# Optimization experiments

Hardware: AMD Instinct MI355X
Metric: run time of the kernel (lower is better)

The kernel has to match this reference:

```python
import jax, jax.numpy as jnp
import numpy as np

B, S, W = 64, 128, 16
E, H = 256, 512
WV, CV, NC = 50000, 128, 20


def _lstm(x, lens, Wih, Whh, b):
    """Masked LSTM over padded sequences.
    x: [N,T,D], lens: [N] int. Returns (ys [N,T,Hd] zeroed past lens, h_last [N,Hd]).
    Gate layout [i,f,g,o] as in PyTorch; b = b_ih + b_hh fused.
    """
    N, T, _ = x.shape
    Hd = Whh.shape[1]

    def step(carry, inp):
        h, c = carry
        xt, t = inp
        z = xt @ Wih.T + h @ Whh.T + b  # [N,4Hd]
        i, f, g, o = jnp.split(z, 4, axis=-1)
        c_new = jax.nn.sigmoid(f) * c + jax.nn.sigmoid(i) * jnp.tanh(g)
        h_new = jax.nn.sigmoid(o) * jnp.tanh(c_new)
        m = (t < lens)[:, None]
        h = jnp.where(m, h_new, h)  # freeze state past sequence end (packed semantics)
        c = jnp.where(m, c_new, c)
        return (h, c), jnp.where(m, h, 0.0)

    h0 = jnp.zeros((N, Hd), x.dtype)
    (h, _), ys = jax.lax.scan(step, (h0, h0), (jnp.swapaxes(x, 0, 1), jnp.arange(T)))
    return jnp.swapaxes(ys, 0, 1), h


def _rev_pad(x, lens):
    """Reverse each sequence within its valid length; padding stays in place."""
    T = x.shape[1]
    t = jnp.arange(T)[None, :]
    idx = jnp.where(t < lens[:, None], lens[:, None] - 1 - t, t)
    return jnp.take_along_axis(x, idx[:, :, None], axis=1)


def setup_inputs() -> dict:
    key = jax.random.key(0)
    ks = jax.random.split(key, 16)
    sc = 0.05
    words = jax.random.randint(ks[0], (B, S), 0, WV)
    words_num = jax.random.randint(ks[1], (B,), 1, S + 1)
    chars = jax.random.randint(ks[2], (B, S, W), 0, CV)
    char_lens = jax.random.randint(ks[3], (B, S), 1, W + 1)
    word_emb = jax.random.normal(ks[4], (WV, E)) * sc
    char_emb = jax.random.normal(ks[5], (CV, E)) * sc
    l0_Wih = jax.random.normal(ks[6], (2, 4 * H, E)) * sc
    l0_Whh = jax.random.normal(ks[7], (2, 4 * H, H)) * sc
    l0_b = jax.random.normal(ks[8], (2, 4 * H)) * sc
    l1_Wih = jax.random.normal(ks[9], (2, 4 * H, 2 * H)) * sc
    l1_Whh = jax.random.normal(ks[10], (2, 4 * H, H)) * sc
    l1_b = jax.random.normal(ks[11], (2, 4 * H)) * sc
    c_Wih = jax.random.normal(ks[12], (4 * (2 * H), E)) * sc
    c_Whh = jax.random.normal(ks[13], (4 * (2 * H), 2 * H)) * sc
    c_b = jax.random.normal(ks[14], (4 * (2 * H),)) * sc
    lin_W = jax.random.normal(ks[15], (NC, 2 * H)) * sc
    lin_b = jnp.zeros((NC,))
    return dict(words=words, words_num=words_num, chars=chars, char_lens=char_lens,
                word_emb=word_emb, char_emb=char_emb,
                l0_Wih=l0_Wih, l0_Whh=l0_Whh, l0_b=l0_b,
                l1_Wih=l1_Wih, l1_Whh=l1_Whh, l1_b=l1_b,
                c_Wih=c_Wih, c_Whh=c_Whh, c_b=c_b,
                lin_W=lin_W, lin_b=lin_b)


def reference(words, words_num, chars, char_lens, word_emb, char_emb,
              l0_Wih, l0_Whh, l0_b, l1_Wih, l1_Whh, l1_b,
              c_Wih, c_Whh, c_b, lin_W, lin_b):
    # word path: embedding + 2-layer bidirectional LSTM (packed -> masked)
    h = word_emb[words]  # [B,S,E]
    for Wih, Whh, b in ((l0_Wih, l0_Whh, l0_b), (l1_Wih, l1_Whh, l1_b)):
        fwd, _ = _lstm(h, words_num, Wih[0], Whh[0], b[0])
        bwd, _ = _lstm(_rev_pad(h, words_num), words_num, Wih[1], Whh[1], b[1])
        h = jnp.concatenate([fwd, _rev_pad(bwd, words_num)], axis=-1)  # [B,S,2H]

    # char path: one batched LSTM over all B*S words (collapses per-sentence loop)
    b_, s_, w_ = chars.shape
    ce = char_emb[chars.reshape(b_ * s_, w_)]  # [B*S,W,E]
    _, hc = _lstm(ce, char_lens.reshape(b_ * s_), c_Wih, c_Whh, c_b)  # final h_n [B*S,2H]
    y = hc.reshape(b_, s_, -1)
    valid = (jnp.arange(s_)[None, :] < words_num[:, None])[..., None]
    y = jnp.where(valid, y, 0.0)  # pad_sequence pads missing words with zeros

    return (h + y) @ lin_W.T + lin_b  # [B,S,NC]
```

## Files before the change

### kernel.cpp

```cpp
#include <hip/hip_runtime.h>
#include <stdint.h>

#define SLEN 128
#define NW 8192
#define WCH 16
#define EDIM 256
#define HDIM 512
#define G4 2048
#define CH 1024
#define CG 4096
#define NCLS 20

typedef __attribute__((ext_vector_type(4))) float f32x4;
typedef __attribute__((ext_vector_type(8))) short s16x8;

__device__ __forceinline__ ushort f2b(float f){
  uint32_t u = __float_as_uint(f);
  return (ushort)((u + 0x7FFFu + ((u>>16)&1u)) >> 16);
}
__device__ __forceinline__ float b2f(ushort s){ return __uint_as_float(((uint32_t)s)<<16); }
__device__ __forceinline__ float sigf(float x){ return 1.f/(1.f+__expf(-x)); }
__device__ __forceinline__ float tanhf_(float x){
  float t = fminf(fmaxf(2.f*x,-30.f),30.f);
  float e = __expf(t);
  return (e-1.f)/(e+1.f);
}

__device__ __forceinline__ void gl16(const ushort* g, ushort* l){
  __builtin_amdgcn_global_load_lds((const __attribute__((address_space(1))) uint32_t*)g,
                                   (__attribute__((address_space(3))) uint32_t*)l, 16, 0, 0);
}

__global__ void k_fill(uint32_t* __restrict__ p, uint32_t v, int n){
  int i = blockIdx.x*256 + threadIdx.x;
  if (i < n) p[i] = v;
}

__global__ void k_cvt(const float* __restrict__ s, ushort* __restrict__ d, int n){
  int i = blockIdx.x*256 + threadIdx.x;
  if (i < n) d[i] = f2b(s[i]);
}

__global__ void k_cwhhp(const float* __restrict__ s, ushort* __restrict__ d){
  int i = blockIdx.x*256 + threadIdx.x;
  int dr = i >> 10, k = i & 1023;
  int nb = dr >> 7, w7 = dr & 127;
  int g = w7 >> 5, wn = (w7>>4)&1, hl = w7&15;
  int h = nb*32 + wn*16 + hl;
  d[i] = f2b(s[(size_t)(g*1024 + h)*1024 + k]);
}

__global__ void k_wwhhp(const float* __restrict__ s, ushort* __restrict__ d){
  int i = blockIdx.x*256 + threadIdx.x;
  int dr = i >> 9, k = i & 511;
  int dir = dr >> 11; int r = dr & 2047;
  int y = r >> 7, w7 = r & 127;
  int g = w7 >> 5, wn = (w7>>4)&1, hl = w7&15;
  int h = y*32 + wn*16 + hl;
  d[i] = f2b(s[((size_t)dir*2048 + g*512 + h)*512 + k]);
}

__global__ void k_emb(const int* __restrict__ words, const float* __restrict__ we,
                      ushort* __restrict__ d){
  int i = blockIdx.x*256 + threadIdx.x;
  int w = i >> 8, e = i & 255;
  d[i] = f2b(we[(size_t)words[w]*EDIM + e]);
}

__global__ void k_cproj(const float* __restrict__ cemb, const float* __restrict__ cwih,
                        const float* __restrict__ cb, float* __restrict__ out){
  int i = blockIdx.x*256 + threadIdx.x;
  int c = i >> 12, p = i & 4095;
  int nb = p >> 7, w7 = p & 127;
  int g = w7>>5, wn = (w7>>4)&1, hl = w7&15;
  int j = g*1024 + nb*32 + wn*16 + hl;
  const float* a = cemb + (size_t)c*EDIM;
  const float* b = cwih + (size_t)j*EDIM;
  float acc = cb[j];
  for (int k=0;k<EDIM;k+=4){
    float4 av = *(const float4*)&a[k]; float4 bv = *(const float4*)&b[k];
    acc += av.x*bv.x + av.y*bv.y + av.z*bv.z + av.w*bv.w;
  }
  out[i] = acc;
}

__global__ void k_hist(const int* __restrict__ wn, const int* __restrict__ cl,
                       int* __restrict__ cnt17){
  int w = blockIdx.x*256 + threadIdx.x; if (w >= NW) return;
  int b = w >> 7, s = w & 127;
  if (s < wn[b]) atomicAdd(&cnt17[cl[w]], 1);
}

__global__ void k_scan(const int* __restrict__ cnt17, int* __restrict__ cnt_step,
                       int* __restrict__ cur){
  if (threadIdx.x==0 && blockIdx.x==0){
    cnt_step[16] = 0;
    for (int t=15;t>=0;t--) cnt_step[t] = cnt_step[t+1] + cnt17[t+1];
    for (int l=1;l<=16;l++) cur[l] = cnt_step[l];
  }
}

__global__ void k_scatter(const int* __restrict__ wn, const int* __restrict__ cl,
                          const int* __restrict__ chars, int* __restrict__ cur,
                          int* __restrict__ inv, int* __restrict__ chperm){
  int w = blockIdx.x*256 + threadIdx.x; if (w >= NW) return;
  int b = w >> 7, s = w & 127;
  if (s < wn[b]){
    int len = cl[w];
    int pos = atomicAdd(&cur[len], 1);
    inv[w] = pos;
    for (int j=0;j<WCH;j++) chperm[pos*WCH + j] = chars[w*WCH + j];
  }
}

template<int EPI>
__global__ __launch_bounds__(256) void k_gemm(
    const ushort* __restrict__ A, int ldA,
    const ushort* __restrict__ Bm, int ldB, size_t bStrideZ,
    ushort* __restrict__ outX, const float* __restrict__ bias,
    size_t oStrideZ, size_t biasStrideZ, int K,
    const int* __restrict__ cnt_step, int tstep,
    const int* __restrict__ chperm, const float* __restrict__ cproj,
    float* __restrict__ ccell, ushort* __restrict__ hcdst)
{
  int cntv = 0;
  if (EPI==1){ cntv = cnt_step[tstep]; if ((int)(blockIdx.x*128) >= cntv) return; }
  __shared__ __align__(16) ushort As[128*64];
  __shared__ __align__(16) ushort Bs[128*64];
  int tid = threadIdx.x, wid = tid>>6, lane = tid&63;
  int wm = wid>>1, wn = wid&1;
  int l15 = lane&15, l4 = lane>>4;
  const ushort* Ab = A + (size_t)blockIdx.x*128*ldA;
  const ushort* Bb = Bm + (size_t)blockIdx.z*bStrideZ + (size_t)blockIdx.y*128*ldB;
  f32x4 acc[4][4];
  #pragma unroll
  for (int i=0;i<4;i++)
    #pragma unroll
    for (int j=0;j<4;j++) acc[i][j] = f32x4{0.f,0.f,0.f,0.f};

  for (int k0=0; k0<K; k0+=64){
    #pragma unroll
    for (int i=0;i<4;i++){
      int fcb = (i*4 + wid)*64;
      int fc = fcb + lane;
      int row = fc>>3, cp = fc&7, c = cp ^ (row&7);
      gl16(Ab + (size_t)row*ldA + k0 + c*8, As + fcb*8);
    }
    #pragma unroll
    for (int i=0;i<4;i++){
      int fcb = (i*4 + wid)*64;
      int fc = fcb + lane;
      int row = fc>>3, cp = fc&7, c = cp ^ (row&7);
      gl16(Bb + (size_t)row*ldB + k0 + c*8, Bs + fcb*8);
    }
    __syncthreads();
    #pragma unroll
    for (int kw=0; kw<2; kw++){
      s16x8 af[4], bfr[4];
      #pragma unroll
      for (int mf=0; mf<4; mf++){
        int r = wm*64 + mf*16 + l15;
        int slot = (kw*4 + l4) ^ (r&7);
        af[mf] = *(const s16x8*)&As[r*64 + slot*8];
      }
      #pragma unroll
      for (int nf=0; nf<4; nf++){
        int r = (EPI==1) ? (nf*32 + wn*16 + l15) : (wn*64 + nf*16 + l15);
        int slot = (kw*4 + l4) ^ (r&7);
        bfr[nf] = *(const s16x8*)&Bs[r*64 + slot*8];
      }
      #pragma unroll
      for (int mf=0; mf<4; mf++)
        #pragma unroll
        for (int nf=0; nf<4; nf++)
          acc[mf][nf] = __builtin_amdgcn_mfma_f32_16x16x32_bf16(af[mf], bfr[nf], acc[mf][nf], 0,0,0);
    }
    __syncthreads();
  }

  if (EPI==0){
    ushort* op = outX + blockIdx.z*oStrideZ;
    const float* bp = bias + blockIdx.z*biasStrideZ;
    #pragma unroll
    for (int mf=0; mf<4; mf++){
      #pragma unroll
      for (int r=0;r<4;r++){
        int row = blockIdx.x*128 + wm*64 + mf*16 + l4*4 + r;
        #pragma unroll
        for (int nf=0;nf<4;nf++){
          int col = blockIdx.y*128 + wn*64 + nf*16 + l15;
          op[(size_t)row*G4 + col] = f2b(acc[mf][nf][r] + bp[col]);
        }
      }
    }
  } else {
    int hb = blockIdx.y*32 + wn*16 + l15;
    #pragma unroll
    for (int mf=0; mf<4; mf++){
      #pragma unroll
      for (int r=0;r<4;r++){
        int row = blockIdx.x*128 + wm*64 + mf*16 + l4*4 + r;
        if (row < cntv){
          int cid = chperm[row*WCH + tstep];
          const float* cp = cproj + (size_t)cid*CG + blockIdx.y*128 + wn*16 + l15;
          float zi = acc[mf][0][r] + cp[0];
          float zf = acc[mf][1][r] + cp[32];
          float zg = acc[mf][2][r] + cp[64];
          float zo = acc[mf][3][r] + cp[96];
          size_t ix = (size_t)row*CH + hb;
          float c = ccell[ix];
          float cn = sigf(zf)*c + sigf(zi)*tanhf_(zg);
          ccell[ix] = cn;
          hcdst[ix] = f2b(sigf(zo)*tanhf_(cn));
        }
      }
    }
  }
}

__global__ __launch_bounds__(256) void k_wstep(
    const ushort* __restrict__ hsrc,
    ushort* __restrict__ hdst,
    float* __restrict__ cst,
    const ushort* __restrict__ X,
    const ushort* __restrict__ Wp,
    const int* __restrict__ lens,
    ushort* __restrict__ outcat,
    int t)
{
  __shared__ __align__(16) ushort As[64*64];
  __shared__ __align__(16) ushort Bs[128*64];
  int tid = threadIdx.x, wid = tid>>6, lane = tid&63;
  int l15 = lane&15, l4 = lane>>4;
  int y = blockIdx.x;
  int dir = blockIdx.y;
  const ushort* Ab = hsrc + (size_t)dir*64*512;
  const ushort* Bb = Wp + ((size_t)dir*2048 + (size_t)y*128)*512;
  f32x4 acc[8];
  #pragma unroll
  for (int n=0;n<8;n++) acc[n] = f32x4{0.f,0.f,0.f,0.f};

  for (int k0=0; k0<512; k0+=64){
    #pragma unroll
    for (int i=0;i<2;i++){
      int fcb = (i*4 + wid)*64;
      int fc = fcb + lane;
      int row = fc>>3, cp = fc&7, c = cp ^ (row&7);
      gl16(Ab + (size_t)row*512 + k0 + c*8, As + fcb*8);
    }
    #pragma unroll
    for (int i=0;i<4;i++){
      int fcb = (i*4 + wid)*64;
      int fc = fcb + lane;
      int row = fc>>3, cp = fc&7, c = cp ^ (row&7);
      gl16(Bb + (size_t)row*512 + k0 + c*8, Bs + fcb*8);
    }
    __syncthreads();
    #pragma unroll
    for (int kw=0; kw<2; kw++){
      s16x8 af;
      {
        int r = wid*16 + l15;
        int slot = (kw*4 + l4) ^ (r&7);
        af = *(const s16x8*)&As[r*64 + slot*8];
      }
      #pragma unroll
      for (int nf=0; nf<8; nf++){
        int r = nf*16 + l15;
        int slot = (kw*4 + l4) ^ (r&7);
        s16x8 bfr = *(const s16x8*)&Bs[r*64 + slot*8];
        acc[nf] = __builtin_amdgcn_mfma_f32_16x16x32_bf16(af, bfr, acc[nf], 0,0,0);
      }
    }
    __syncthreads();
  }

  int b0 = wid*16 + l4*4;
  int lenv[4], posv[4];
  #pragma unroll
  for (int r=0;r<4;r++){
    int len = lens[b0+r];
    lenv[r] = len;
    posv[r] = dir ? (len-1-t) : t;
  }
  #pragma unroll
  for (int wn=0;wn<2;wn++){
    int h = y*32 + wn*16 + l15;
    #pragma unroll
    for (int r=0;r<4;r++){
      int b = b0 + r;
      size_t hix = ((size_t)dir*64 + b)*512 + h;
      ushort hnew;
      if (t < lenv[r]){
        size_t xbase = ((size_t)dir*NW + (size_t)b*SLEN + posv[r])*G4 + h;
        float zi = acc[0+wn][r] + b2f(X[xbase]);
        float zf = acc[2+wn][r] + b2f(X[xbase + 512]);
        float zg = acc[4+wn][r] + b2f(X[xbase + 1024]);
        float zo = acc[6+wn][r] + b2f(X[xbase + 1536]);
        size_t cix = ((size_t)dir*512 + h)*64 + b;
        float c = cst[cix];
        float cn = sigf(zf)*c + sigf(zi)*tanhf_(zg);
        cst[cix] = cn;
        float hv = sigf(zo)*tanhf_(cn);
        hnew = f2b(hv);
        outcat[((size_t)b*SLEN + posv[r])*1024 + dir*HDIM + h] = hnew;
      } else {
        hnew = hsrc[hix];
      }
      hdst[hix] = hnew;
    }
  }
}

__global__ void k_gather(const ushort* __restrict__ hc0, const ushort* __restrict__ hc1,
                         const int* __restrict__ inv, const int* __restrict__ cl,
                         ushort* __restrict__ ycat){
  int i = blockIdx.x*256 + threadIdx.x;
  if (i >= NW*128) return;
  int w = i >> 7, seg = i & 127;
  int iv = inv[w];
  ulonglong2 z; z.x = 0; z.y = 0;
  if (iv >= 0){
    const ushort* src = (((cl[w]-1)&1) ? hc0 : hc1) + (size_t)iv*CH + seg*8;
    z = *(const ulonglong2*)src;
  }
  *(ulonglong2*)(ycat + (size_t)w*CH + seg*8) = z;
}

__global__ __launch_bounds__(256) void k_final(
    const ushort* __restrict__ h1cat, const ushort* __restrict__ ycat,
    const float* __restrict__ lw, const float* __restrict__ lb,
    float* __restrict__ out)
{
  int i = blockIdx.x*256 + threadIdx.x;
  if (i >= NW*NCLS) return;
  int w = i / NCLS, o = i - w*NCLS;
  const ushort* hr = h1cat + (size_t)w*1024;
  const ushort* yr = ycat  + (size_t)w*1024;
  const float* wr = lw + (size_t)o*1024;
  float acc = lb[o];
  for (int k=0;k<1024;k+=4){
    float4 wv = *(const float4*)&wr[k];
    ushort4 a4 = *(const ushort4*)&hr[k];
    ushort4 b4 = *(const ushort4*)&yr[k];
    acc += (b2f(a4.x)+b2f(b4.x))*wv.x + (b2f(a4.y)+b2f(b4.y))*wv.y
         + (b2f(a4.z)+b2f(b4.z))*wv.z + (b2f(a4.w)+b2f(b4.w))*wv.w;
  }
  out[i] = acc;
}

extern "C" void kernel_launch(void* const* d_in, const int* in_sizes, int n_in,
                              void* d_out, int out_size, void* d_ws, size_t ws_size,
                              hipStream_t stream)
{
  const int*   words = (const int*)d_in[0];
  const int*   wnum  = (const int*)d_in[1];
  const int*   chars = (const int*)d_in[2];
  const int*   clens = (const int*)d_in[3];
  const float* wemb  = (const float*)d_in[4];
  const float* cemb  = (const float*)d_in[5];
  const float* l0Wih = (const float*)d_in[6];
  const float* l0Whh = (const float*)d_in[7];
  const float* l0b   = (const float*)d_in[8];
  const float* l1Wih = (const float*)d_in[9];
  const float* l1Whh = (const float*)d_in[10];
  const float* l1b   = (const float*)d_in[11];
  const float* cWih  = (const float*)d_in[12];
  const float* cWhh  = (const float*)d_in[13];
  const float* cb    = (const float*)d_in[14];
  const float* linW  = (const float*)d_in[15];
  const float* linb  = (const float*)d_in[16];
  float* out = (float*)d_out;

  char* base = (char*)d_ws;
  const size_t MB = (size_t)1<<20;
  ushort* hc0    = (ushort*)(base);
  ushort* hc1    = (ushort*)(base + 16*MB);
  float*  ccell  = (float*) (base + 32*MB);
  ushort* X      = (ushort*)(base);
  ushort* cwp    = (ushort*)(base + 64*MB);
  ushort* l1w    = (ushort*)(base + 64*MB);
  float*  cproj  = (float*) (base + 72*MB);
  int*    chperm = (int*)   (base + 74*MB);
  ushort* embw   = (ushort*)(base + 72*MB);
  ushort* w1p    = (ushort*)(base + 72*MB);
  ushort* ycat   = (ushort*)(base + 76*MB);
  ushort* h0cat  = (ushort*)(base + 92*MB);
  ushort* h1cat  = (ushort*)(base + 92*MB);
  ushort* l0w    = (ushort*)(base + 108*MB);
  ushort* w0p    = (ushort*)(base + 110*MB);
  ushort* hA     = (ushort*)(base + 114*MB);
  ushort* hB     = (ushort*)(base + 114*MB + 128*1024);
  float*  cw     = (float*) (base + 114*MB + 256*1024);
  int*    inv    = (int*)   (base + 114*MB + 512*1024);
  int*    cnt17  = (int*)   (base + 114*MB + 544*1024);
  int*    cntstep= (int*)   (base + 114*MB + 545*1024);
  int*    cur    = (int*)   (base + 114*MB + 546*1024);

  k_fill<<<1, 256, 0, stream>>>((uint32_t*)cnt17, 0u, 17);
  k_fill<<<(NW+255)/256, 256, 0, stream>>>((uint32_t*)inv, 0xFFFFFFFFu, NW);
  k_fill<<<(NW*CH/2+255)/256, 256, 0, stream>>>((uint32_t*)hc0, 0u, NW*CH/2);
  k_fill<<<(NW*CH+255)/256, 256, 0, stream>>>((uint32_t*)ccell, 0u, NW*CH);
  k_cwhhp<<<(CG*CH)/256, 256, 0, stream>>>(cWhh, cwp);
  k_cproj<<<(128*CG)/256, 256, 0, stream>>>(cemb, cWih, cb, cproj);
  k_hist<<<NW/256, 256, 0, stream>>>(wnum, clens, cnt17);
  k_scan<<<1, 1, 0, stream>>>(cnt17, cntstep, cur);
  k_scatter<<<NW/256, 256, 0, stream>>>(wnum, clens, chars, cur, inv, chperm);

  for (int t=0;t<WCH;t++){
    const ushort* hs = (t&1)? hc1 : hc0;
    ushort*       hd = (t&1)? hc0 : hc1;
    k_gemm<1><<<dim3(64,32,1), 256, 0, stream>>>(hs, CH, cwp, CH, 0,
        nullptr, nullptr, 0, 0, CH,
        cntstep, t, chperm, cproj, ccell, hd);
  }
  k_gather<<<(NW*128+255)/256, 256, 0, stream>>>(hc0, hc1, inv, clens, ycat);

  k_cvt<<<(2*G4*EDIM+255)/256, 256, 0, stream>>>(l0Wih, l0w, 2*G4*EDIM);
  k_cvt<<<(2*G4*1024+255)/256, 256, 0, stream>>>(l1Wih, l1w, 2*G4*1024);
  k_wwhhp<<<(2*G4*HDIM)/256, 256, 0, stream>>>(l0Whh, w0p);
  k_emb<<<(NW*EDIM)/256, 256, 0, stream>>>(words, wemb, embw);
  k_fill<<<(NW*512+255)/256, 256, 0, stream>>>((uint32_t*)h0cat, 0u, NW*512);
  k_fill<<<(32768+255)/256, 256, 0, stream>>>((uint32_t*)hA, 0u, 32768);
  k_fill<<<(65536+255)/256, 256, 0, stream>>>((uint32_t*)cw, 0u, 65536);

  k_gemm<0><<<dim3(64,16,2), 256, 0, stream>>>(embw, EDIM, l0w, EDIM, (size_t)G4*EDIM,
      X, l0b, (size_t)NW*G4, (size_t)G4, EDIM,
      nullptr, 0, nullptr, nullptr, nullptr, nullptr);

  k_wwhhp<<<(2*G4*HDIM)/256, 256, 0, stream>>>(l1Whh, w1p);

  for (int t=0;t<SLEN;t++){
    const ushort* hs = (t&1)? hB : hA;
    ushort*       hd = (t&1)? hA : hB;
    k_wstep<<<dim3(16,2), 256, 0, stream>>>(hs, hd, cw, X, w0p, wnum, h0cat, t);
  }

  k_fill<<<(32768+255)/256, 256, 0, stream>>>((uint32_t*)hA, 0u, 32768);
  k_fill<<<(65536+255)/256, 256, 0, stream>>>((uint32_t*)cw, 0u, 65536);

  k_gemm<0><<<dim3(64,16,2), 256, 0, stream>>>(h0cat, 1024, l1w, 1024, (size_t)G4*1024,
      X, l1b, (size_t)NW*G4, (size_t)G4, 1024,
      nullptr, 0, nullptr, nullptr, nullptr, nullptr);

  k_fill<<<(NW*512+255)/256, 256, 0, stream>>>((uint32_t*)h1cat, 0u, NW*512);

  for (int t=0;t<SLEN;t++){
    const ushort* hs = (t&1)? hB : hA;
    ushort*       hd = (t&1)? hA : hB;
    k_wstep<<<dim3(16,2), 256, 0, stream>>>(hs, hd, cw, X, w1p, wnum, h1cat, t);
  }

  k_final<<<(NW*NCLS+255)/256, 256, 0, stream>>>(h1cat, ycat, linW, linb, out);
}
```

Before: 4.837 ms.

## Replace per-step word LSTM launches with persistent kernel and grid barrier

Each word-LSTM layer now runs as one persistent 32-block kernel instead of 128 separate launches. Each block keeps its 128-row slice of Whh resident in LDS (128 KB), holds the cell state in registers, and synchronises the 16 blocks of each direction through an atomic counter barrier in global memory after every timestep. This removes launch overhead and the repeated reload of the weights per step. The price is a spin-wait barrier that depends on all 32 blocks being co-resident, plus high LDS use per block.

Result: faster. 4.432 ms (-8.4%).

```diff
diff --git a/kernel.cpp b/kernel.cpp
--- a/kernel.cpp
+++ b/kernel.cpp
@@ -218,97 +218,117 @@
   }
 }
 
-__global__ __launch_bounds__(256) void k_wstep(
-    const ushort* __restrict__ hsrc,
-    ushort* __restrict__ hdst,
-    float* __restrict__ cst,
+__global__ __launch_bounds__(256) void k_wrec(
+    ushort* __restrict__ hbuf,
     const ushort* __restrict__ X,
     const ushort* __restrict__ Wp,
     const int* __restrict__ lens,
     ushort* __restrict__ outcat,
-    int t)
+    int* __restrict__ bar)
 {
+  __shared__ __align__(16) ushort Ws[8*128*64];
   __shared__ __align__(16) ushort As[64*64];
-  __shared__ __align__(16) ushort Bs[128*64];
   int tid = threadIdx.x, wid = tid>>6, lane = tid&63;
   int l15 = lane&15, l4 = lane>>4;
-  int y = blockIdx.x;
-  int dir = blockIdx.y;
-  const ushort* Ab = hsrc + (size_t)dir*64*512;
-  const ushort* Bb = Wp + ((size_t)dir*2048 + (size_t)y*128)*512;
-  f32x4 acc[8];
+  int y = blockIdx.x & 15, dir = blockIdx.x >> 4;
+  const ushort* Wb = Wp + ((size_t)dir*2048 + (size_t)y*128)*512;
+
   #pragma unroll
-  for (int n=0;n<8;n++) acc[n] = f32x4{0.f,0.f,0.f,0.f};
-
-  for (int k0=0; k0<512; k0+=64){
-    #pragma unroll
-    for (int i=0;i<2;i++){
-      int fcb = (i*4 + wid)*64;
-      int fc = fcb + lane;
-      int row = fc>>3, cp = fc&7, c = cp ^ (row&7);
-      gl16(Ab + (size_t)row*512 + k0 + c*8, As + fcb*8);
-    }
+  for (int kt=0; kt<8; ++kt)
     #pragma unroll
     for (int i=0;i<4;i++){
       int fcb = (i*4 + wid)*64;
       int fc = fcb + lane;
       int row = fc>>3, cp = fc&7, c = cp ^ (row&7);
-      gl16(Bb + (size_t)row*512 + k0 + c*8, Bs + fcb*8);
-    }
+      gl16(Wb + (size_t)row*512 + kt*64 + c*8, Ws + kt*8192 + fcb*8);
+    }
+  asm volatile("s_waitcnt vmcnt(0)" ::: "memory");
+  __builtin_amdgcn_sched_barrier(0);
+  __builtin_amdgcn_s_barrier();
+
+  int b0 = wid*16 + l4*4;
+  int lenv[4];
+  #pragma unroll
+  for (int r=0;r<4;r++) lenv[r] = lens[b0+r];
+  float  cacc[2][4];
+  ushort hprev[2][4];
+  #pragma unroll
+  for (int wn=0;wn<2;wn++)
+    #pragma unroll
+    for (int r=0;r<4;r++){ cacc[wn][r]=0.f; hprev[wn][r]=0; }
+
+  int* mybar = bar + dir;
+
+  for (int t=0;t<SLEN;t++){
+    const ushort* hsrc = hbuf + ((size_t)((t&1)*2 + dir))*32768;
+    ushort*       hdst = hbuf + ((size_t)((((t&1)^1))*2 + dir))*32768;
+    f32x4 acc[8];
+    #pragma unroll
+    for (int n=0;n<8;n++) acc[n] = f32x4{0.f,0.f,0.f,0.f};
+
+    for (int kt=0; kt<8; ++kt){
+      #pragma unroll
+      for (int i=0;i<2;i++){
+        int fcb = (i*4 + wid)*64;
+        int fc = fcb + lane;
+        int row = fc>>3, cp = fc&7, c = cp ^ (row&7);
+        gl16(hsrc + (size_t)row*512 + kt*64 + c*8, As + fcb*8);
+      }
+      asm volatile("s_waitcnt vmcnt(0)" ::: "memory");
+      __builtin_amdgcn_sched_barrier(0);
+      __builtin_amdgcn_s_barrier();
+      #pragma unroll
+      for (int kw=0; kw<2; kw++){
+        s16x8 af;
+        { int r = wid*16 + l15; int slot = (kw*4 + l4) ^ (r&7);
+          af = *(const s16x8*)&As[r*64 + slot*8]; }
+        #pragma unroll
+        for (int nf=0; nf<8; nf++){
+          int r = nf*16 + l15; int slot = (kw*4 + l4) ^ (r&7);
+          s16x8 bfr = *(const s16x8*)&Ws[kt*8192 + r*64 + slot*8];
+          acc[nf] = __builtin_amdgcn_mfma_f32_16x16x32_bf16(af, bfr, acc[nf], 0,0,0);
+        }
+      }
+      __builtin_amdgcn_s_barrier();
+    }
+
+    #pragma unroll
+    for (int wn=0;wn<2;wn++){
+      int h = y*32 + wn*16 + l15;
+      #pragma unroll
+      for (int r=0;r<4;r++){
+        int b = b0 + r;
+        ushort hnew;
+        if (t < lenv[r]){
+          int pos = dir ? (lenv[r]-1-t) : t;
+          size_t xbase = ((size_t)dir*NW + (size_t)b*SLEN + pos)*G4 + h;
+          float zi = acc[0+wn][r] + b2f(X[xbase]);
+          float zf = acc[2+wn][r] + b2f(X[xbase + 512]);
+          float zg = acc[4+wn][r] + b2f(X[xbase + 1024]);
+          float zo = acc[6+wn][r] + b2f(X[xbase + 1536]);
+          float cn = sigf(zf)*cacc[wn][r] + sigf(zi)*tanhf_(zg);
+          cacc[wn][r] = cn;
+          float hv = sigf(zo)*tanhf_(cn);
+          hnew = f2b(hv);
+          outcat[((size_t)b*SLEN + pos)*1024 + dir*HDIM + h] = hnew;
+        } else {
+          hnew = hprev[wn][r];
+        }
+        hprev[wn][r] = hnew;
+        hdst[(size_t)b*512 + h] = hnew;
+      }
+    }
+
     __syncthreads();
-    #pragma unroll
-    for (int kw=0; kw<2; kw++){
-      s16x8 af;
-      {
-        int r = wid*16 + l15;
-        int slot = (kw*4 + l4) ^ (r&7);
-        af = *(const s16x8*)&As[r*64 + slot*8];
-      }
-      #pragma unroll
-      for (int nf=0; nf<8; nf++){
-        int r = nf*16 + l15;
-        int slot = (kw*4 + l4) ^ (r&7);
-        s16x8 bfr = *(const s16x8*)&Bs[r*64 + slot*8];
-        acc[nf] = __builtin_amdgcn_mfma_f32_16x16x32_bf16(af, bfr, acc[nf], 0,0,0);
-      }
+    if (tid==0){
+      __threadfence();
+      __hip_atomic_fetch_add(mybar, 1, __ATOMIC_RELEASE, __HIP_MEMORY_SCOPE_AGENT);
+      int tgt = 16*(t+1);
+      while (__hip_atomic_load(mybar, __ATOMIC_ACQUIRE, __HIP_MEMORY_SCOPE_AGENT) < tgt)
+        __builtin_amdgcn_s_sleep(8);
+      __threadfence();
     }
     __syncthreads();
-  }
-
-  int b0 = wid*16 + l4*4;
-  int lenv[4], posv[4];
-  #pragma unroll
-  for (int r=0;r<4;r++){
-    int len = lens[b0+r];
-    lenv[r] = len;
-    posv[r] = dir ? (len-1-t) : t;
-  }
-  #pragma unroll
-  for (int wn=0;wn<2;wn++){
-    int h = y*32 + wn*16 + l15;
-    #pragma unroll
-    for (int r=0;r<4;r++){
-      int b = b0 + r;
-      size_t hix = ((size_t)dir*64 + b)*512 + h;
-      ushort hnew;
-      if (t < lenv[r]){
-        size_t xbase = ((size_t)dir*NW + (size_t)b*SLEN + posv[r])*G4 + h;
-        float zi = acc[0+wn][r] + b2f(X[xbase]);
-        float zf = acc[2+wn][r] + b2f(X[xbase + 512]);
-        float zg = acc[4+wn][r] + b2f(X[xbase + 1024]);
-        float zo = acc[6+wn][r] + b2f(X[xbase + 1536]);
-        size_t cix = ((size_t)dir*512 + h)*64 + b;
-        float c = cst[cix];
-        float cn = sigf(zf)*c + sigf(zi)*tanhf_(zg);
-        cst[cix] = cn;
-        float hv = sigf(zo)*tanhf_(cn);
-        hnew = f2b(hv);
-        outcat[((size_t)b*SLEN + posv[r])*1024 + dir*HDIM + h] = hnew;
-      } else {
-        hnew = hsrc[hix];
-      }
-      hdst[hix] = hnew;
-    }
   }
 }
 
@@ -389,9 +409,8 @@
   ushort* h1cat  = (ushort*)(base + 92*MB);
   ushort* l0w    = (ushort*)(base + 108*MB);
   ushort* w0p    = (ushort*)(base + 110*MB);
-  ushort* hA     = (ushort*)(base + 114*MB);
-  ushort* hB     = (ushort*)(base + 114*MB + 128*1024);
-  float*  cw     = (float*) (base + 114*MB + 256*1024);
+  ushort* hbuf   = (ushort*)(base + 114*MB);
+  int*    bar    = (int*)   (base + 114*MB + 256*1024);
   int*    inv    = (int*)   (base + 114*MB + 512*1024);
   int*    cnt17  = (int*)   (base + 114*MB + 544*1024);
   int*    cntstep= (int*)   (base + 114*MB + 545*1024);
@@ -421,8 +440,8 @@
   k_wwhhp<<<(2*G4*HDIM)/256, 256, 0, stream>>>(l0Whh, w0p);
   k_emb<<<(NW*EDIM)/256, 256, 0, stream>>>(words, wemb, embw);
   k_fill<<<(NW*512+255)/256, 256, 0, stream>>>((uint32_t*)h0cat, 0u, NW*512);
-  k_fill<<<(32768+255)/256, 256, 0, stream>>>((uint32_t*)hA, 0u, 32768);
-  k_fill<<<(65536+255)/256, 256, 0, stream>>>((uint32_t*)cw, 0u, 65536);
+  k_fill<<<(32768+255)/256, 256, 0, stream>>>((uint32_t*)hbuf, 0u, 32768);
+  k_fill<<<1, 256, 0, stream>>>((uint32_t*)bar, 0u, 2);
 
   k_gemm<0><<<dim3(64,16,2), 256, 0, stream>>>(embw, EDIM, l0w, EDIM, (size_t)G4*EDIM,
       X, l0b, (size_t)NW*G4, (size_t)G4, EDIM,
@@ -430,26 +449,17 @@
 
   k_wwhhp<<<(2*G4*HDIM)/256, 256, 0, stream>>>(l1Whh, w1p);
 
-  for (int t=0;t<SLEN;t++){
-    const ushort* hs = (t&1)? hB : hA;
-    ushort*       hd = (t&1)? hA : hB;
-    k_wstep<<<dim3(16,2), 256, 0, stream>>>(hs, hd, cw, X, w0p, wnum, h0cat, t);
-  }
-
-  k_fill<<<(32768+255)/256, 256, 0, stream>>>((uint32_t*)hA, 0u, 32768);
-  k_fill<<<(65536+255)/256, 256, 0, stream>>>((uint32_t*)cw, 0u, 65536);
+  k_wrec<<<32, 256, 0, stream>>>(hbuf, X, w0p, wnum, h0cat, bar);
 
   k_gemm<0><<<dim3(64,16,2), 256, 0, stream>>>(h0cat, 1024, l1w, 1024, (size_t)G4*1024,
       X, l1b, (size_t)NW*G4, (size_t)G4, 1024,
       nullptr, 0, nullptr, nullptr, nullptr, nullptr);
 
   k_fill<<<(NW*512+255)/256, 256, 0, stream>>>((uint32_t*)h1cat, 0u, NW*512);
-
-  for (int t=0;t<SLEN;t++){
-    const ushort* hs = (t&1)? hB : hA;
-    ushort*       hd = (t&1)? hA : hB;
-    k_wstep<<<dim3(16,2), 256, 0, stream>>>(hs, hd, cw, X, w1p, wnum, h1cat, t);
-  }
+  k_fill<<<(32768+255)/256, 256, 0, stream>>>((uint32_t*)hbuf, 0u, 32768);
+  k_fill<<<1, 256, 0, stream>>>((uint32_t*)bar, 0u, 2);
+
+  k_wrec<<<32, 256, 0, stream>>>(hbuf, X, w1p, wnum, h1cat, bar);
 
   k_final<<<(NW*NCLS+255)/256, 256, 0, stream>>>(h1cat, ycat, linW, linb, out);
 }
```
